# Kernel tuning notes

Hardware: AMD Instinct MI355X
Metric: run time of the kernel (lower is better)

## Reference

```python
import jax, jax.numpy as jnp
import numpy as np

C_M, C_Z, C_H = 256, 128, 32
N_SEQ, N_RES = 128, 256
EPS = 1e-3


def setup_inputs() -> dict:
    key = jax.random.key(0)
    ks = jax.random.split(key, 8)
    s = 0.02
    return {
        "m": jax.random.normal(ks[0], (N_SEQ, N_RES, C_M), dtype=jnp.float32),
        "mask": jnp.ones((N_SEQ, N_RES), dtype=jnp.float32),
        "ln_gamma": jnp.ones((C_M,), dtype=jnp.float32),
        "ln_beta": jnp.zeros((C_M,), dtype=jnp.float32),
        "W1": jax.random.normal(ks[1], (C_M, C_H), dtype=jnp.float32) * s,
        "b1": jnp.zeros((C_H,), dtype=jnp.float32),
        "W2": jax.random.normal(ks[2], (C_M, C_H), dtype=jnp.float32) * s,
        "b2": jnp.zeros((C_H,), dtype=jnp.float32),
        "Wout": jax.random.normal(ks[3], (C_H * C_H, C_Z), dtype=jnp.float32) * s,
        "bout": jnp.zeros((C_Z,), dtype=jnp.float32),
    }


def reference(m, mask, ln_gamma, ln_beta, W1, b1, W2, b2, Wout, bout):
    # LayerNorm over last dim (c_m)
    mu = jnp.mean(m, axis=-1, keepdims=True)
    var = jnp.var(m, axis=-1, keepdims=True)
    ln = (m - mu) * jax.lax.rsqrt(var + 1e-5) * ln_gamma + ln_beta

    mk = mask[..., None]                       # [S, R, 1]
    a = (ln @ W1 + b1) * mk                    # [S, R, c_h]
    b = (ln @ W2 + b2) * mk                    # [S, R, c_h]

    # outer-product mean: contract over the MSA seq dim
    outer = jnp.einsum('sbc,sde->bdce', a, b)  # [R, R, c_h, c_h]
    outer = outer.reshape(N_RES, N_RES, C_H * C_H)
    outer = outer @ Wout + bout                # [R, R, c_z]

    norm = jnp.einsum('sb,sd->bd', mask, mask)[..., None] + EPS  # [R, R, 1]
    return outer / norm
```

## Files before the change

### kernel.cpp

```cpp
#include <hip/hip_runtime.h>

#define S_DIM 128
#define R_DIM 256
#define CM 256
#define CH 32
#define CZ 128

typedef short bf16x8 __attribute__((ext_vector_type(8)));
typedef float f32x4 __attribute__((ext_vector_type(4)));
typedef unsigned short ushort_t;

static __device__ __forceinline__ unsigned short f2bf(float f) {
  union { float f; unsigned u; } v; v.f = f;
  unsigned r = v.u + 0x7FFF + ((v.u >> 16) & 1);
  return (unsigned short)(r >> 16);
}
static __device__ __forceinline__ float bf2f(unsigned short b) {
  union { unsigned u; float f; } v; v.u = ((unsigned)b) << 16;
  return v.f;
}

static __device__ __forceinline__ void gload_lds16(const void* g, void* l) {
  __builtin_amdgcn_global_load_lds(
      (const __attribute__((address_space(1))) void*)g,
      (__attribute__((address_space(3))) void*)l, 16, 0, 0);
}

__global__ __launch_bounds__(256) void prep_kernel(
    const float* __restrict__ W1, const float* __restrict__ b1,
    const float* __restrict__ W2, const float* __restrict__ b2,
    const float* __restrict__ gamma, const float* __restrict__ beta,
    ushort_t* __restrict__ pwT, float* __restrict__ SGCB) {
  int c = blockIdx.x;
  int cm = threadIdx.x;
  __shared__ float red[8];
  float w = (c < 32) ? W1[cm * 32 + c] : W2[cm * 32 + (c - 32)];
  unsigned short pw = f2bf(gamma[cm] * w);
  pwT[c * 256 + cm] = pw;
  float sg = bf2f(pw), cb = beta[cm] * w;
  for (int o = 32; o > 0; o >>= 1) {
    sg += __shfl_down(sg, o);
    cb += __shfl_down(cb, o);
  }
  if ((cm & 63) == 0) { red[cm >> 6] = sg; red[4 + (cm >> 6)] = cb; }
  __syncthreads();
  if (cm == 0) {
    float s = red[0] + red[1] + red[2] + red[3];
    float q = red[4] + red[5] + red[6] + red[7];
    SGCB[c] = s;
    SGCB[64 + c] = q + ((c < 32) ? b1[c] : b2[c - 32]);
  }
}

__global__ __launch_bounds__(256) void proj_kernel(
    const float* __restrict__ m, const float* __restrict__ mask,
    const ushort_t* __restrict__ pwT, const float* __restrict__ SGCB,
    const float* __restrict__ Wout,
    ushort_t* __restrict__ aB, ushort_t* __restrict__ bB,
    ushort_t* __restrict__ WT, float* __restrict__ normT) {
  extern __shared__ char pmem[];
  int blk = blockIdx.x;
  int t = threadIdx.x;

  if (blk >= 512) {
    if (blk < 544) {
      int e = blk - 512;
      float* wS = (float*)pmem;
#pragma unroll
      for (int i = 0; i < 16; ++i) {
        int idx = i * 256 + t;
        int cc = idx >> 7, z = idx & 127;
        wS[cc * 129 + z] = Wout[(size_t)(cc * 32 + e) * CZ + z];
      }
      __syncthreads();
#pragma unroll
      for (int i = 0; i < 16; ++i) {
        int idx = i * 256 + t;
        int z = idx >> 5, cc = idx & 31;
        WT[(size_t)z * 1024 + e * 32 + cc] = f2bf(wS[cc * 129 + z]);
      }
    } else {
      int b = blk - 544;
      float ps = 0.f;
      for (int s = 0; s < S_DIM; ++s)
        ps += mask[s * R_DIM + b] * mask[s * R_DIM + t];
      normT[(size_t)b * R_DIM + t] = ps + 1e-3f;
    }
    return;
  }

  ushort_t* mhS = (ushort_t*)pmem;
  ushort_t* mlS = (ushort_t*)(pmem + 32768);
  __shared__ float s1S[64], s2S[64], mkS[64];

  int r = blk >> 1, sh = blk & 1;

  {
    int s = t >> 2, q = t & 3;
    const float* src = m + ((size_t)((sh * 64 + s) * R_DIM + r)) * CM + q * 64;
    float s1 = 0.f, s2 = 0.f;
#pragma unroll
    for (int i = 0; i < 8; ++i) {
      float4 v0 = *(const float4*)(src + i * 8);
      float4 v1 = *(const float4*)(src + i * 8 + 4);
      float xs[8] = {v0.x, v0.y, v0.z, v0.w, v1.x, v1.y, v1.z, v1.w};
      union { ushort_t h[8]; float4 f; } H, L;
#pragma unroll
      for (int j = 0; j < 8; ++j) {
        float x = xs[j];
        s1 += x; s2 += x * x;
        unsigned short hh = f2bf(x);
        H.h[j] = hh;
        L.h[j] = f2bf(x - bf2f(hh));
      }
      int ch = q * 8 + i, phys = ch ^ (s & 7);
      *(float4*)&mhS[s * 256 + phys * 8] = H.f;
      *(float4*)&mlS[s * 256 + phys * 8] = L.f;
    }
    s1 += __shfl_xor(s1, 1); s1 += __shfl_xor(s1, 2);
    s2 += __shfl_xor(s2, 1); s2 += __shfl_xor(s2, 2);
    if (q == 0) {
      s1S[s] = s1; s2S[s] = s2;
      mkS[s] = mask[(sh * 64 + s) * R_DIM + r];
    }
  }
  __syncthreads();

  int wave = t >> 6, lane = t & 63, l16 = lane & 15, lk = lane >> 4;
  int wm = wave >> 1, wn = wave & 1;
  f32x4 zero4 = {0.f, 0.f, 0.f, 0.f};
  f32x4 acc[2][2];
  acc[0][0] = zero4; acc[0][1] = zero4; acc[1][0] = zero4; acc[1][1] = zero4;

#pragma unroll
  for (int kstep = 0; kstep < 8; ++kstep) {
    int mm = kstep * 4 + lk;
    bf16x8 bw[2];
#pragma unroll
    for (int nf = 0; nf < 2; ++nf) {
      int cr = wn * 32 + nf * 16 + l16;
      bw[nf] = *(const bf16x8*)(pwT + cr * 256 + mm * 8);
    }
#pragma unroll
    for (int mf = 0; mf < 2; ++mf) {
      int srow = wm * 32 + mf * 16 + l16;
      int phys = mm ^ (srow & 7);
      bf16x8 ah = *(const bf16x8*)&mhS[srow * 256 + phys * 8];
      bf16x8 al = *(const bf16x8*)&mlS[srow * 256 + phys * 8];
#pragma unroll
      for (int nf = 0; nf < 2; ++nf)
        acc[mf][nf] = __builtin_amdgcn_mfma_f32_16x16x32_bf16(ah, bw[nf], acc[mf][nf], 0, 0, 0);
#pragma unroll
      for (int nf = 0; nf < 2; ++nf)
        acc[mf][nf] = __builtin_amdgcn_mfma_f32_16x16x32_bf16(al, bw[nf], acc[mf][nf], 0, 0, 0);
    }
  }

#pragma unroll
  for (int nf = 0; nf < 2; ++nf) {
    int c = wn * 32 + nf * 16 + l16;
    float sgv = SGCB[c], cbv = SGCB[64 + c];
#pragma unroll
    for (int mf = 0; mf < 2; ++mf) {
      union { ushort_t u[4]; uint2 v; } pk;
#pragma unroll
      for (int j = 0; j < 4; ++j) {
        int s = wm * 32 + mf * 16 + lk * 4 + j;
        float mu = s1S[s] * (1.0f / CM);
        float var = s2S[s] * (1.0f / CM) - mu * mu;
        float ri = rsqrtf(var + 1e-5f);
        float val = (ri * (acc[mf][nf][j] - mu * sgv) + cbv) * mkS[s];
        pk.u[j] = f2bf(val);
      }
      int sg0 = sh * 64 + wm * 32 + mf * 16 + lk * 4;
      if (c < 32)
        *(uint2*)&aB[((size_t)(r * 32 + c)) * S_DIM + sg0] = pk.v;
      else
        *(uint2*)&bB[((size_t)(r * 32 + (c - 32))) * S_DIM + sg0] = pk.v;
    }
  }
}

__global__ __launch_bounds__(512, 2) void outer_mfma_kernel(
    const ushort_t* __restrict__ aB, const ushort_t* __restrict__ bB,
    const ushort_t* __restrict__ WT, const float* __restrict__ normT,
    const float* __restrict__ bout, float* __restrict__ out) {
  extern __shared__ char smem[];
  __shared__ float nrm[64];
  int t = threadIdx.x;
  int lane = t & 63, wave = t >> 6;
  int l16 = lane & 15, lk = lane >> 4;

  int bid = blockIdx.x;
  int swz = (bid & 7) * 128 + (bid >> 3);
  int b0 = (swz >> 5) * 8, d0 = (swz & 31) * 8;

  {
    const ushort_t* srcA = aB + (size_t)b0 * 32 * S_DIM;
    const ushort_t* srcB = bB + (size_t)d0 * 32 * S_DIM;
#pragma unroll
    for (int i = 0; i < 16; ++i) {
      int cid = t + i * 512;
      int q = cid & 4095, row = q >> 4, pm = q & 15;
      int lg = pm ^ (row & 7);
      const ushort_t* src = (cid & 4096) ? srcB : srcA;
      gload_lds16(src + (size_t)row * S_DIM + lg * 8, smem + cid * 16);
    }
  }

  if (t < 64) nrm[t] = normT[(size_t)(b0 + (t >> 3)) * R_DIM + d0 + (t & 7)];

  __syncthreads();

  int wm = wave >> 1, wn = wave & 1;
  f32x4 zero4 = {0.f, 0.f, 0.f, 0.f};
  f32x4 acc[4][8];
#pragma unroll
  for (int i = 0; i < 4; ++i)
#pragma unroll
    for (int j = 0; j < 8; ++j) acc[i][j] = zero4;

#pragma unroll
  for (int ks = 0; ks < 4; ++ks) {
    int mm = ks * 4 + lk;
    bf16x8 af[4], bf[8];
#pragma unroll
    for (int r = 0; r < 4; ++r) {
      int row = wm * 64 + r * 16 + l16;
      af[r] = *(const bf16x8*)(smem + row * 256 + ((mm ^ (row & 7)) << 4));
    }
#pragma unroll
    for (int c = 0; c < 8; ++c) {
      int row = wn * 128 + c * 16 + l16;
      bf[c] = *(const bf16x8*)(smem + 65536 + row * 256 + ((mm ^ (row & 7)) << 4));
    }
#pragma unroll
    for (int r = 0; r < 4; ++r)
#pragma unroll
      for (int c = 0; c < 8; ++c)
        acc[r][c] = __builtin_amdgcn_mfma_f32_16x16x32_bf16(af[r], bf[c], acc[r][c], 0, 0, 0);
  }
  __syncthreads();

  int z = wave * 16 + l16;
  const ushort_t* wtz = WT + (size_t)z * 1024;
  bf16x8 wtpre0 = *(const bf16x8*)(wtz + lk * 8);
  bf16x8 wtpre1 = *(const bf16x8*)(wtz + 32 + lk * 8);

#define TSTORE(rr, cc_)                                                        \
  {                                                                            \
    int Mrow = wm * 64 + (rr) * 16 + lk * 4;                                   \
    int bsub = Mrow >> 5, cc = Mrow & 31;                                      \
    int Ncol = wn * 128 + (cc_) * 16 + l16;                                    \
    int dsub = Ncol >> 5, e = Ncol & 31;                                       \
    int p = bsub * 8 + dsub;                                                   \
    int chunk = e * 4 + (cc >> 3);                                             \
    int pch = chunk ^ ((chunk >> 3) & 7) ^ (p & 7);                            \
    union { ushort_t u[4]; uint2 v; } pk;                                      \
    pk.u[0] = f2bf(acc[rr][cc_][0]);                                           \
    pk.u[1] = f2bf(acc[rr][cc_][1]);                                           \
    pk.u[2] = f2bf(acc[rr][cc_][2]);                                           \
    pk.u[3] = f2bf(acc[rr][cc_][3]);                                           \
    *(uint2*)(smem + p * 2048 + pch * 16 + (cc & 4) * 2) = pk.v;               \
  }

#pragma unroll
  for (int r = 0; r < 4; ++r)
#pragma unroll
    for (int ci = 0; ci < 4; ++ci) TSTORE(r, ci * 2);
  __syncthreads();

#pragma unroll
  for (int r = 0; r < 4; ++r)
#pragma unroll
    for (int ci = 0; ci < 4; ++ci) TSTORE(r, ci * 2 + 1);
#undef TSTORE

#define ARD(ks, pf)                                                            \
  (*(const bf16x8*)(smem + ((pf) * 16 + l16) * 2048 +                          \
                    ((((ks) * 4 + lk) ^ ((((ks) * 4 + lk) >> 3) & 7) ^         \
                      (((pf) * 16 + l16) & 7))                                 \
                     << 4)))

  f32x4 oc[4];
#pragma unroll
  for (int i = 0; i < 4; ++i) oc[i] = zero4;

  bf16x8 wtb[4];
  wtb[0] = wtpre0;
  wtb[1] = wtpre1;
  wtb[2] = *(const bf16x8*)(wtz + 64 + lk * 8);
  wtb[3] = *(const bf16x8*)(wtz + 96 + lk * 8);

  bf16x8 a_cur[4], a_nxt[4];
#pragma unroll
  for (int pf = 0; pf < 4; ++pf) a_cur[pf] = ARD(0, pf);

#pragma unroll
  for (int ks = 0; ks < 16; ++ks) {
    bf16x8 bfr = wtb[ks & 3];
    if (ks + 4 < 32)
      wtb[ks & 3] = *(const bf16x8*)(wtz + (ks + 4) * 32 + lk * 8);
    if (ks + 1 < 16) {
#pragma unroll
      for (int pf = 0; pf < 4; ++pf) a_nxt[pf] = ARD(ks + 1, pf);
    }
#pragma unroll
    for (int pf = 0; pf < 4; ++pf)
      oc[pf] = __builtin_amdgcn_mfma_f32_16x16x32_bf16(a_cur[pf], bfr, oc[pf], 0, 0, 0);
#pragma unroll
    for (int pf = 0; pf < 4; ++pf) a_cur[pf] = a_nxt[pf];
  }
  __syncthreads();

#pragma unroll
  for (int pf = 0; pf < 4; ++pf) a_cur[pf] = ARD(16, pf);
#pragma unroll
  for (int ks = 16; ks < 32; ++ks) {
    bf16x8 bfr = wtb[ks & 3];
    if (ks + 4 < 32)
      wtb[ks & 3] = *(const bf16x8*)(wtz + (ks + 4) * 32 + lk * 8);
    if (ks + 1 < 32) {
#pragma unroll
      for (int pf = 0; pf < 4; ++pf) a_nxt[pf] = ARD(ks + 1, pf);
    }
#pragma unroll
    for (int pf = 0; pf < 4; ++pf)
      oc[pf] = __builtin_amdgcn_mfma_f32_16x16x32_bf16(a_cur[pf], bfr, oc[pf], 0, 0, 0);
#pragma unroll
    for (int pf = 0; pf < 4; ++pf) a_cur[pf] = a_nxt[pf];
  }
#undef ARD

  float bo = bout[z];
#pragma unroll
  for (int pf = 0; pf < 4; ++pf) {
#pragma unroll
    for (int j = 0; j < 4; ++j) {
      int p = pf * 16 + lk * 4 + j;
      int b = b0 + (p >> 3), d = d0 + (p & 7);
      out[((size_t)(b * R_DIM + d)) * CZ + z] = (oc[pf][j] + bo) / nrm[p];
    }
  }
}

extern "C" void kernel_launch(void* const* d_in, const int* in_sizes, int n_in,
                              void* d_out, int out_size, void* d_ws, size_t ws_size,
                              hipStream_t stream) {
  const float* m     = (const float*)d_in[0];
  const float* mask  = (const float*)d_in[1];
  const float* gamma = (const float*)d_in[2];
  const float* beta  = (const float*)d_in[3];
  const float* W1    = (const float*)d_in[4];
  const float* b1    = (const float*)d_in[5];
  const float* W2    = (const float*)d_in[6];
  const float* b2    = (const float*)d_in[7];
  const float* Wout  = (const float*)d_in[8];
  const float* bout  = (const float*)d_in[9];
  float* out = (float*)d_out;

  char* ws = (char*)d_ws;
  ushort_t* aB    = (ushort_t*)ws;
  ushort_t* bB    = (ushort_t*)(ws + (size_t)2 * 1024 * 1024);
  ushort_t* WT    = (ushort_t*)(ws + (size_t)4 * 1024 * 1024);
  ushort_t* pwT   = (ushort_t*)(ws + (size_t)4352 * 1024);
  float*    SGCB  = (float*)   (ws + (size_t)4416 * 1024);
  float*    normT = (float*)   (ws + (size_t)4480 * 1024);

  hipFuncSetAttribute((const void*)outer_mfma_kernel,
                      hipFuncAttributeMaxDynamicSharedMemorySize, 131072);
  hipFuncSetAttribute((const void*)proj_kernel,
                      hipFuncAttributeMaxDynamicSharedMemorySize, 65536);

  prep_kernel<<<64, 256, 0, stream>>>(W1, b1, W2, b2, gamma, beta, pwT, SGCB);
  proj_kernel<<<800, 256, 65536, stream>>>(m, mask, pwT, SGCB, Wout,
                                           aB, bB, WT, normT);
  outer_mfma_kernel<<<1024, 512, 131072, stream>>>(aB, bB, WT, normT, bout, out);
}
```

Measured before the change: 81.58 us.

## Retile output projection waves as 2x2 pair-by-z tiles and precompute reciprocal norm

The second-stage GEMM is retiled so each wave covers 32 pairs by 32 output channels (two A fragments times two Wout fragments) instead of 64 pairs by 16 channels. This halves the LDS A-fragment reads per MFMA but doubles the Wout global/L2 register loads per wave. The norm buffer now stores reciprocals so the epilogue multiplies instead of divides. This relies on nrm being read from normT, which is not visible here.

Result: slower. 105.1 us (+28.9%).

```diff
diff --git a/kernel.cpp b/kernel.cpp
--- a/kernel.cpp
+++ b/kernel.cpp
@@ -84,7 +84,7 @@
       float ps = 0.f;
       for (int s = 0; s < S_DIM; ++s)
         ps += mask[s * R_DIM + b] * mask[s * R_DIM + t];
-      normT[(size_t)b * R_DIM + t] = ps + 1e-3f;
+      normT[(size_t)b * R_DIM + t] = 1.0f / (ps + 1e-3f);
     }
     return;
   }
@@ -242,10 +242,16 @@
   }
   __syncthreads();
 
-  int z = wave * 16 + l16;
-  const ushort_t* wtz = WT + (size_t)z * 1024;
-  bf16x8 wtpre0 = *(const bf16x8*)(wtz + lk * 8);
-  bf16x8 wtpre1 = *(const bf16x8*)(wtz + 32 + lk * 8);
+  int wp = wave >> 2, wz = wave & 3;
+  int z0 = wz * 32 + l16;
+  const ushort_t* wtz0 = WT + (size_t)z0 * 1024;
+  const ushort_t* wtz1 = wtz0 + (size_t)16 * 1024;
+
+  bf16x8 wt0[4], wt1[4];
+  wt0[0] = *(const bf16x8*)(wtz0 + lk * 8);
+  wt1[0] = *(const bf16x8*)(wtz1 + lk * 8);
+  wt0[1] = *(const bf16x8*)(wtz0 + 32 + lk * 8);
+  wt1[1] = *(const bf16x8*)(wtz1 + 32 + lk * 8);
 
 #define TSTORE(rr, cc_)                                                        \
   {                                                                            \
@@ -277,69 +283,76 @@
 #undef TSTORE
 
 #define ARD(ks, pf)                                                            \
-  (*(const bf16x8*)(smem + ((pf) * 16 + l16) * 2048 +                          \
+  (*(const bf16x8*)(smem + (wp * 32 + (pf) * 16 + l16) * 2048 +                \
                     ((((ks) * 4 + lk) ^ ((((ks) * 4 + lk) >> 3) & 7) ^         \
-                      (((pf) * 16 + l16) & 7))                                 \
+                      ((wp * 32 + (pf) * 16 + l16) & 7))                       \
                      << 4)))
 
-  f32x4 oc[4];
-#pragma unroll
-  for (int i = 0; i < 4; ++i) oc[i] = zero4;
-
-  bf16x8 wtb[4];
-  wtb[0] = wtpre0;
-  wtb[1] = wtpre1;
-  wtb[2] = *(const bf16x8*)(wtz + 64 + lk * 8);
-  wtb[3] = *(const bf16x8*)(wtz + 96 + lk * 8);
-
-  bf16x8 a_cur[4], a_nxt[4];
-#pragma unroll
-  for (int pf = 0; pf < 4; ++pf) a_cur[pf] = ARD(0, pf);
+  f32x4 oc[2][2];
+  oc[0][0] = zero4; oc[0][1] = zero4; oc[1][0] = zero4; oc[1][1] = zero4;
+
+  wt0[2] = *(const bf16x8*)(wtz0 + 64 + lk * 8);
+  wt1[2] = *(const bf16x8*)(wtz1 + 64 + lk * 8);
+  wt0[3] = *(const bf16x8*)(wtz0 + 96 + lk * 8);
+  wt1[3] = *(const bf16x8*)(wtz1 + 96 + lk * 8);
+
+  bf16x8 a_cur[2], a_nxt[2];
+#pragma unroll
+  for (int pf = 0; pf < 2; ++pf) a_cur[pf] = ARD(0, pf);
 
 #pragma unroll
   for (int ks = 0; ks < 16; ++ks) {
-    bf16x8 bfr = wtb[ks & 3];
-    if (ks + 4 < 32)
-      wtb[ks & 3] = *(const bf16x8*)(wtz + (ks + 4) * 32 + lk * 8);
+    bf16x8 br0 = wt0[ks & 3], br1 = wt1[ks & 3];
+    if (ks + 4 < 32) {
+      wt0[ks & 3] = *(const bf16x8*)(wtz0 + (ks + 4) * 32 + lk * 8);
+      wt1[ks & 3] = *(const bf16x8*)(wtz1 + (ks + 4) * 32 + lk * 8);
+    }
     if (ks + 1 < 16) {
 #pragma unroll
-      for (int pf = 0; pf < 4; ++pf) a_nxt[pf] = ARD(ks + 1, pf);
-    }
-#pragma unroll
-    for (int pf = 0; pf < 4; ++pf)
-      oc[pf] = __builtin_amdgcn_mfma_f32_16x16x32_bf16(a_cur[pf], bfr, oc[pf], 0, 0, 0);
-#pragma unroll
-    for (int pf = 0; pf < 4; ++pf) a_cur[pf] = a_nxt[pf];
-  }
-  __syncthreads();
-
-#pragma unroll
-  for (int pf = 0; pf < 4; ++pf) a_cur[pf] = ARD(16, pf);
+      for (int pf = 0; pf < 2; ++pf) a_nxt[pf] = ARD(ks + 1, pf);
+    }
+#pragma unroll
+    for (int pf = 0; pf < 2; ++pf) {
+      oc[pf][0] = __builtin_amdgcn_mfma_f32_16x16x32_bf16(a_cur[pf], br0, oc[pf][0], 0, 0, 0);
+      oc[pf][1] = __builtin_amdgcn_mfma_f32_16x16x32_bf16(a_cur[pf], br1, oc[pf][1], 0, 0, 0);
+    }
+    a_cur[0] = a_nxt[0]; a_cur[1] = a_nxt[1];
+  }
+  __syncthreads();
+
+#pragma unroll
+  for (int pf = 0; pf < 2; ++pf) a_cur[pf] = ARD(16, pf);
 #pragma unroll
   for (int ks = 16; ks < 32; ++ks) {
-    bf16x8 bfr = wtb[ks & 3];
-    if (ks + 4 < 32)
-      wtb[ks & 3] = *(const bf16x8*)(wtz + (ks + 4) * 32 + lk * 8);
+    bf16x8 br0 = wt0[ks & 3], br1 = wt1[ks & 3];
+    if (ks + 4 < 32) {
+      wt0[ks & 3] = *(const bf16x8*)(wtz0 + (ks + 4) * 32 + lk * 8);
+      wt1[ks & 3] = *(const bf16x8*)(wtz1 + (ks + 4) * 32 + lk * 8);
+    }
     if (ks + 1 < 32) {
 #pragma unroll
-      for (int pf = 0; pf < 4; ++pf) a_nxt[pf] = ARD(ks + 1, pf);
-    }
-#pragma unroll
-    for (int pf = 0; pf < 4; ++pf)
-      oc[pf] = __builtin_amdgcn_mfma_f32_16x16x32_bf16(a_cur[pf], bfr, oc[pf], 0, 0, 0);
-#pragma unroll
-    for (int pf = 0; pf < 4; ++pf) a_cur[pf] = a_nxt[pf];
+      for (int pf = 0; pf < 2; ++pf) a_nxt[pf] = ARD(ks + 1, pf);
+    }
+#pragma unroll
+    for (int pf = 0; pf < 2; ++pf) {
+      oc[pf][0] = __builtin_amdgcn_mfma_f32_16x16x32_bf16(a_cur[pf], br0, oc[pf][0], 0, 0, 0);
+      oc[pf][1] = __builtin_amdgcn_mfma_f32_16x16x32_bf16(a_cur[pf], br1, oc[pf][1], 0, 0, 0);
+    }
+    a_cur[0] = a_nxt[0]; a_cur[1] = a_nxt[1];
   }
 #undef ARD
 
-  float bo = bout[z];
-#pragma unroll
-  for (int pf = 0; pf < 4; ++pf) {
+  float bo0 = bout[z0], bo1 = bout[z0 + 16];
+#pragma unroll
+  for (int pf = 0; pf < 2; ++pf) {
 #pragma unroll
     for (int j = 0; j < 4; ++j) {
-      int p = pf * 16 + lk * 4 + j;
+      int p = wp * 32 + pf * 16 + lk * 4 + j;
       int b = b0 + (p >> 3), d = d0 + (p & 7);
-      out[((size_t)(b * R_DIM + d)) * CZ + z] = (oc[pf][j] + bo) / nrm[p];
+      float rn = nrm[p];
+      size_t base = ((size_t)(b * R_DIM + d)) * CZ;
+      out[base + z0]      = (oc[pf][0][j] + bo0) * rn;
+      out[base + z0 + 16] = (oc[pf][1][j] + bo1) * rn;
     }
   }
 }
```
